# Kernel tuning notes

Measured on AMD Instinct MI355X. Metric: run time of the kernel, lower is better.

The kernel has to match this reference:

```python
import jax, jax.numpy as jnp
import numpy as np

EMBED = 128   # embed_dims
NCAM = 6      # cameras per sample
FH, FW = 6, 12  # per-camera feature map size (same at every scale here)
THRESH = 0.01   # opacity threshold (GaussianRenderer.threshold)
SIZES = [25, 50, 100, 200]  # int(200 * 2**(s - 4 + 1)) for s in 0..3


def setup_inputs() -> dict:
    key = jax.random.key(0)
    ks = jax.random.split(key, 16)
    inp = {}
    for s in range(4):
        kf, km, ku, ko = ks[4 * s:4 * s + 4]
        inp[f"features{s}"] = jax.random.normal(kf, (NCAM, EMBED, FH, FW), dtype=jnp.float32)
        # means in the BEV range (-50, 50) meters
        inp[f"means{s}"] = jax.random.uniform(km, (NCAM, FH, FW, 3), minval=-50.0, maxval=50.0, dtype=jnp.float32)
        # PSD 3x3 uncertainty (covariance) per gaussian
        L = jax.random.normal(ku, (NCAM, FH, FW, 3, 3), dtype=jnp.float32)
        inp[f"uncert{s}"] = jnp.einsum('...ij,...kj->...ik', L, L) * 2.0 + jnp.eye(3, dtype=jnp.float32)
        inp[f"opac{s}"] = jax.random.uniform(ko, (NCAM, 1, FH, FW), dtype=jnp.float32)
    inp["b"] = 1
    inp["n"] = NCAM
    return inp


def _render_scale(feat, mean, unc, opac, H, W, b):
    # feat: [(b n), d, h, w]; mean: [(b n), h, w, 3]; unc: [(b n), h, w, 3, 3]; opac: [(b n), 1, h, w]
    bn, d, h, w = feat.shape
    N = (bn // b) * h * w
    f = feat.transpose(0, 2, 3, 1).reshape(b, N, d)          # b (n h w) d
    m = mean.reshape(b, N, 3)
    c9 = unc.reshape(b, N, 9)                                # flatten(-2,-1)
    # pack [xx, xy, xz, yy, yz, zz] then clamp(min=1)
    c6 = jnp.maximum(jnp.concatenate([c9[:, :, 0:3], c9[:, :, 4:6], c9[:, :, 8:9]], axis=-1), 1.0)
    o = opac.transpose(0, 2, 3, 1).reshape(b, N)

    # orthographic BEV projection: pix_row = -sh*y + H/2, pix_col = -sw*x + W/2
    sh = H / 100.0
    sw = W / 100.0
    pr = -sh * m[:, :, 1] + H / 2.0
    pc = -sw * m[:, :, 0] + W / 2.0

    # 2D covariance = J Sigma J^T with J = [[0,-sh,0],[-sw,0,0]]; +0.3 pixel dilation
    va = sh * sh * c6[:, :, 3] + 0.3   # row-row (from Sigma_yy)
    vb = sh * sw * c6[:, :, 1]         # row-col (from Sigma_xy)
    vc = sw * sw * c6[:, :, 0] + 0.3   # col-col (from Sigma_xx)
    det = va * vc - vb * vb

    rows = jnp.arange(H, dtype=feat.dtype)
    cols = jnp.arange(W, dtype=feat.dtype)
    dr = pr[:, :, None, None] - rows[None, None, :, None]    # [b,N,H,1]
    dc = pc[:, :, None, None] - cols[None, None, None, :]    # [b,N,1,W]

    power = (-0.5 * (vc[:, :, None, None] * dr * dr + va[:, :, None, None] * dc * dc)
             + vb[:, :, None, None] * dr * dc) / det[:, :, None, None]   # [b,N,H,W]

    keep = (o > THRESH) & (det > 0.0)                        # mask-gather expressed as alpha zeroing
    alpha = jnp.minimum(0.99, o[:, :, None, None] * jnp.exp(jnp.minimum(power, 0.0)))
    alpha = jnp.where(keep[:, :, None, None] & (power <= 0.0) & (alpha >= 1.0 / 255.0), alpha, 0.0)

    # front-to-back alpha compositing in gaussian order (depth is identically 0 in BEV)
    A = alpha.reshape(b, N, H * W)
    T = jnp.cumprod(1.0 - A, axis=1)
    T_excl = jnp.concatenate([jnp.ones_like(T[:, :1]), T[:, :-1]], axis=1)
    out = jnp.einsum('bnp,bnd->bdp', A * T_excl, f).reshape(b, d, H, W)  # bg color is zeros

    num_g = (o > THRESH).astype(feat.dtype).sum(1).mean()
    return out, num_g


def reference(features0, features1, features2, features3,
              means0, means1, means2, means3,
              uncert0, uncert1, uncert2, uncert3,
              opac0, opac1, opac2, opac3, b, n):
    feats = [features0, features1, features2, features3]
    means = [means0, means1, means2, means3]
    uncs = [uncert0, uncert1, uncert2, uncert3]
    ops = [opac0, opac1, opac2, opac3]
    outs = []
    num_gaussians = jnp.float32(0.0)
    for s in range(4):
        o, g = _render_scale(feats[s], means[s], uncs[s], ops[s], SIZES[s], SIZES[s], b)
        outs.append(o)
        num_gaussians = num_gaussians + g
    return (outs[0], outs[1], outs[2], outs[3], num_gaussians)
```

## Files before the change

kernel.cpp:

```cpp
#include <hip/hip_runtime.h>

#define NCAM   6
#define FHW    72
#define EMBED  128
#define NG     432
#define THRESH 0.01f
#define AMIN   (1.0f/255.0f)
#define NTILES 891
#define TC     432

struct Args {
    const float* feat[4];
    const float* mean[4];
    const float* unc[4];
    const float* opac[4];
};

__device__ __forceinline__ void tile_decode(int g, int& s, int& H, int& band, int& chunk)
{
    int tb;
    if (g < 14)       { s = 0; H = 25;  tb = g;       chunk = tb & 1;  band = tb >> 1; }
    else if (g < 66)  { s = 1; H = 50;  tb = g - 14;  chunk = tb & 3;  band = tb >> 2; }
    else if (g < 241) { s = 2; H = 100; tb = g - 66;  band = tb / 7;   chunk = tb - band * 7; }
    else              { s = 3; H = 200; tb = g - 241; band = tb / 13;  chunk = tb - band * 13; }
}

__global__ __launch_bounds__(256) void prep(Args a, float* __restrict__ ft,
                                            int* __restrict__ tlen,
                                            float4* __restrict__ p4a,
                                            float4* __restrict__ p4b,
                                            float* __restrict__ out)
{
    int b = blockIdx.x, t = threadIdx.x;
    if (b < NTILES) {
        __shared__ int s_cnt[8];
        int g = b;
        int s, H, band, chunk;
        tile_decode(g, s, H, band, chunk);
        int lane = t & 63, wv = t >> 6;
        float sh = H * 0.01f;
        float r0f = (float)(band * 4), r1f = (float)min(band * 4 + 3, H - 1);
        float c0f = (float)(chunk * 16), c1f = (float)min(chunk * 16 + 15, H - 1);
        const float* mean = a.mean[s];
        const float* unc  = a.unc[s];
        const float* opac = a.opac[s];

        bool v_act[2]; int v_rnk[2];
        float v_pr[2], v_pc[2], v_qa[2], v_qb[2], v_qc[2], v_ok[2];
        #pragma unroll
        for (int pp = 0; pp < 2; pp++) {
            int j = pp * 256 + t;
            bool act = false;
            float pr = 0.f, pc = 0.f, qa = 0.f, qb = 0.f, qc = 0.f, ok = 0.f;
            if (j < NG) {
                float m0 = mean[j*3+0], m1 = mean[j*3+1];
                float u00 = fmaxf(unc[j*9+0], 1.f);
                float u01 = fmaxf(unc[j*9+1], 1.f);
                float u11 = fmaxf(unc[j*9+4], 1.f);
                float op = opac[j];
                pr = -sh*m1 + H*0.5f;
                pc = -sh*m0 + H*0.5f;
                float va = sh*sh*u11 + 0.3f;
                float vb = sh*sh*u01;
                float vc = sh*sh*u00 + 0.3f;
                float det = va*vc - vb*vb;
                if (op > THRESH && det > 0.f) {
                    float inv = 1.f/det;
                    qa = 0.5f*vc*inv;
                    qc = 0.5f*va*inv;
                    qb = vb*inv;
                    ok = op;
                    float thr = __logf(255.f*op);
                    float Rr = sqrtf(2.f*va*thr) + 1e-2f;
                    float Rc = sqrtf(2.f*vc*thr) + 1e-2f;
                    act = (pr >= r0f-Rr) && (pr <= r1f+Rr) &&
                          (pc >= c0f-Rc) && (pc <= c1f+Rc);
                }
            }
            unsigned long long m = __ballot(act);
            v_act[pp] = act;
            v_rnk[pp] = __popcll(m & ((1ull << lane) - 1ull));
            v_pr[pp]=pr; v_pc[pp]=pc; v_qa[pp]=qa; v_qb[pp]=qb; v_qc[pp]=qc; v_ok[pp]=ok;
            if (lane == 0) s_cnt[pp*4 + wv] = __popcll(m);
        }
        __syncthreads();
        int c8[8];
        #pragma unroll
        for (int i = 0; i < 8; i++) c8[i] = s_cnt[i];
        int len = 0;
        #pragma unroll
        for (int i = 0; i < 8; i++) len += c8[i];
        #pragma unroll
        for (int pp = 0; pp < 2; pp++) {
            int slot = pp*4 + wv;
            int pre = 0;
            #pragma unroll
            for (int i = 0; i < 8; i++) pre += (i < slot) ? c8[i] : 0;
            if (v_act[pp]) {
                int idx = g*TC + pre + v_rnk[pp];
                int j = pp * 256 + t;
                unsigned off = (unsigned)((s*NG + j) * EMBED);
                p4a[idx] = make_float4(v_pr[pp], v_pc[pp], v_qa[pp], v_qb[pp]);
                p4b[idx] = make_float4(v_qc[pp], v_ok[pp], __uint_as_float(off), 0.f);
            }
        }
        if (t == 0) tlen[g] = len;
    } else if (b < NTILES + 24) {
        __shared__ float l[EMBED * 73];
        int sc = b - NTILES;
        int s = sc / NCAM, cam = sc - s * NCAM;
        const float* src = a.feat[s] + cam * (EMBED * FHW);
        for (int i = t; i < EMBED * FHW; i += 256) {
            int d = i / FHW, hw = i - d * FHW;
            l[d * 73 + hw] = src[i];
        }
        __syncthreads();
        float* dst = ft + (s * NG + cam * FHW) * EMBED;
        for (int e = t; e < EMBED * FHW; e += 256) {
            int hw = e >> 7, d = e & 127;
            dst[hw * EMBED + d] = l[d * 73 + hw];
        }
    } else {
        __shared__ float red[256];
        float c = 0.f;
        for (int s = 0; s < 4; s++)
            for (int i = t; i < NG; i += 256)
                c += (a.opac[s][i] > THRESH) ? 1.f : 0.f;
        red[t] = c;
        __syncthreads();
        for (int st = 128; st > 0; st >>= 1) {
            if (t < st) red[t] += red[t + st];
            __syncthreads();
        }
        if (t == 0) out[6800000] = red[0];
    }
}

__global__ __launch_bounds__(256) void render(const float* __restrict__ ft,
                                              const int* __restrict__ tlen,
                                              const float4* __restrict__ p4a,
                                              const float4* __restrict__ p4b,
                                              float* __restrict__ out)
{
    __shared__ float s_T[4][64];
    __shared__ float s_part[3][64][33];

    int bb = blockIdx.x, t = threadIdx.x;
    int g = bb >> 2, chq = bb & 3;
    int s, H, band, chunk;
    tile_decode(g, s, H, band, chunk);
    int P = H * H;
    float* o = out + ((s == 0) ? 0 : (s == 1) ? 80000 : (s == 2) ? 400000 : 1680000);
    int lane = t & 63;
    int wv = __builtin_amdgcn_readfirstlane(t >> 6);
    int ch0 = chq * 32;
    int len = tlen[g];
    int qlen = (len + 3) >> 2;
    int k0 = wv * qlen, k1 = min(k0 + qlen, len);
    int base = g * TC;
    int row = band*4 + (lane >> 4), col = chunk*16 + (lane & 15);
    float frow = (float)row, fcol = (float)col;

    float acc[32];
    #pragma unroll
    for (int i = 0; i < 32; i++) acc[i] = 0.f;
    float T = 1.f;

    if (k0 < k1) {
        float4 A = p4a[base + k0];
        float4 B = p4b[base + k0];
        for (int k = k0; k < k1; k++) {
            unsigned off = __builtin_amdgcn_readfirstlane(__float_as_uint(B.z));
            const float* fr = ft + off + ch0;
            float4 f0 = *reinterpret_cast<const float4*>(fr);
            float4 f1 = *reinterpret_cast<const float4*>(fr + 4);
            float4 f2 = *reinterpret_cast<const float4*>(fr + 8);
            float4 f3 = *reinterpret_cast<const float4*>(fr + 12);
            float4 f4 = *reinterpret_cast<const float4*>(fr + 16);
            float4 f5 = *reinterpret_cast<const float4*>(fr + 20);
            float4 f6 = *reinterpret_cast<const float4*>(fr + 24);
            float4 f7 = *reinterpret_cast<const float4*>(fr + 28);
            int kn = (k + 1 < k1) ? k + 1 : k;
            float4 An = p4a[base + kn];
            float4 Bn = p4b[base + kn];
            float dr = A.x - frow, dc = A.y - fcol;
            float pw = A.w*dr*dc - A.z*dr*dr - B.x*dc*dc;
            float aL = 0.f;
            if (pw <= 0.f) {
                aL = fminf(B.y * __expf(pw), 0.99f);
                aL = (aL >= AMIN) ? aL : 0.f;
            }
            float w = aL * T;
            T *= (1.f - aL);
            acc[0]  += w * f0.x; acc[1]  += w * f0.y; acc[2]  += w * f0.z; acc[3]  += w * f0.w;
            acc[4]  += w * f1.x; acc[5]  += w * f1.y; acc[6]  += w * f1.z; acc[7]  += w * f1.w;
            acc[8]  += w * f2.x; acc[9]  += w * f2.y; acc[10] += w * f2.z; acc[11] += w * f2.w;
            acc[12] += w * f3.x; acc[13] += w * f3.y; acc[14] += w * f3.z; acc[15] += w * f3.w;
            acc[16] += w * f4.x; acc[17] += w * f4.y; acc[18] += w * f4.z; acc[19] += w * f4.w;
            acc[20] += w * f5.x; acc[21] += w * f5.y; acc[22] += w * f5.z; acc[23] += w * f5.w;
            acc[24] += w * f6.x; acc[25] += w * f6.y; acc[26] += w * f6.z; acc[27] += w * f6.w;
            acc[28] += w * f7.x; acc[29] += w * f7.y; acc[30] += w * f7.z; acc[31] += w * f7.w;
            A = An; B = Bn;
        }
    }

    s_T[wv][lane] = T;
    __syncthreads();
    if (wv > 0) {
        float pref = s_T[0][lane];
        if (wv > 1) pref *= s_T[1][lane];
        if (wv > 2) pref *= s_T[2][lane];
        #pragma unroll
        for (int i = 0; i < 32; i++)
            s_part[wv-1][lane][i] = acc[i] * pref;
    }
    __syncthreads();
    if (wv == 0 && row < H && col < H) {
        int pp = row * H + col;
        #pragma unroll
        for (int i = 0; i < 32; i++) {
            float v = acc[i] + s_part[0][lane][i] + s_part[1][lane][i]
                             + s_part[2][lane][i];
            o[(ch0 + i) * P + pp] = v;
        }
    }
}

extern "C" void kernel_launch(void* const* d_in, const int* in_sizes, int n_in,
                              void* d_out, int out_size, void* d_ws, size_t ws_size,
                              hipStream_t stream)
{
    Args a;
    for (int s = 0; s < 4; s++) {
        a.feat[s] = (const float*)d_in[4 * s + 0];
        a.mean[s] = (const float*)d_in[4 * s + 1];
        a.unc[s]  = (const float*)d_in[4 * s + 2];
        a.opac[s] = (const float*)d_in[4 * s + 3];
    }
    float* ws = (float*)d_ws;
    float*  ft   = ws;
    int*    tlen = (int*)(ws + 221184);
    float4* p4a  = (float4*)(ws + 222080);
    float4* p4b  = p4a + NTILES * TC;

    prep<<<NTILES + 24 + 1, 256, 0, stream>>>(a, ft, tlen, p4a, p4b, (float*)d_out);
    render<<<NTILES * 4, 256, 0, stream>>>(ft, tlen, p4a, p4b, (float*)d_out);
}
```

Before: 27.12 us.

## Rebalance render work split across k-sections and channel quarters per scale

```diff
diff --git a/kernel.cpp b/kernel.cpp
--- a/kernel.cpp
+++ b/kernel.cpp
@@ -136,27 +136,34 @@
     }
 }
 
-__global__ __launch_bounds__(256) void render(const float* __restrict__ ft,
+__global__ __launch_bounds__(512) void render(const float* __restrict__ ft,
                                               const int* __restrict__ tlen,
                                               const float4* __restrict__ p4a,
                                               const float4* __restrict__ p4b,
                                               float* __restrict__ out)
 {
-    __shared__ float s_T[4][64];
-    __shared__ float s_part[3][64][33];
+    __shared__ float s_T[8][64];
+    __shared__ float s_part[7][64][33];
 
     int bb = blockIdx.x, t = threadIdx.x;
-    int g = bb >> 2, chq = bb & 3;
+    int lane = t & 63;
+    int wv = __builtin_amdgcn_readfirstlane(t >> 6);
+    int g, chq, ksec, ksections;
+    bool longscale;
+    if (bb < 264) {
+        longscale = true;  g = bb >> 2;        chq = bb & 3;  ksec = wv;      ksections = 8;
+    } else {
+        longscale = false; g = 66 + (bb - 264); chq = wv >> 1; ksec = wv & 1;  ksections = 2;
+    }
+
     int s, H, band, chunk;
     tile_decode(g, s, H, band, chunk);
     int P = H * H;
     float* o = out + ((s == 0) ? 0 : (s == 1) ? 80000 : (s == 2) ? 400000 : 1680000);
-    int lane = t & 63;
-    int wv = __builtin_amdgcn_readfirstlane(t >> 6);
+    int len = tlen[g];
+    int ql = (len + ksections - 1) / ksections;
+    int k0 = min(ksec * ql, len), k1 = min(k0 + ql, len);
     int ch0 = chq * 32;
-    int len = tlen[g];
-    int qlen = (len + 3) >> 2;
-    int k0 = wv * qlen, k1 = min(k0 + qlen, len);
     int base = g * TC;
     int row = band*4 + (lane >> 4), col = chunk*16 + (lane & 15);
     float frow = (float)row, fcol = (float)col;
@@ -204,24 +211,51 @@
         }
     }
 
-    s_T[wv][lane] = T;
-    __syncthreads();
-    if (wv > 0) {
-        float pref = s_T[0][lane];
-        if (wv > 1) pref *= s_T[1][lane];
-        if (wv > 2) pref *= s_T[2][lane];
-        #pragma unroll
-        for (int i = 0; i < 32; i++)
-            s_part[wv-1][lane][i] = acc[i] * pref;
-    }
-    __syncthreads();
-    if (wv == 0 && row < H && col < H) {
-        int pp = row * H + col;
-        #pragma unroll
-        for (int i = 0; i < 32; i++) {
-            float v = acc[i] + s_part[0][lane][i] + s_part[1][lane][i]
-                             + s_part[2][lane][i];
-            o[(ch0 + i) * P + pp] = v;
+    bool inb = (row < H) && (col < H);
+    int pp = row * H + col;
+
+    if (longscale) {
+        s_T[wv][lane] = T;
+        __syncthreads();
+        if (wv > 0) {
+            float pref = s_T[0][lane];
+            #pragma unroll
+            for (int q = 1; q < 7; q++)
+                if (q < wv) pref *= s_T[q][lane];
+            #pragma unroll
+            for (int i = 0; i < 32; i++)
+                s_part[wv-1][lane][i] = acc[i] * pref;
+        }
+        __syncthreads();
+        if (wv == 0 && inb) {
+            #pragma unroll
+            for (int i = 0; i < 32; i++) {
+                float v = acc[i];
+                #pragma unroll
+                for (int q = 0; q < 7; q++) v += s_part[q][lane][i];
+                o[(ch0 + i) * P + pp] = v;
+            }
+        }
+    } else {
+        if (wv == 0) {
+            #pragma unroll
+            for (int i = 0; i < 64; i += 64) ;
+            s_T[0][lane] = T;
+        }
+        __syncthreads();
+        if (ksec == 1) {
+            float pref = s_T[0][lane];
+            #pragma unroll
+            for (int i = 0; i < 32; i++)
+                s_part[chq][lane][i] = acc[i] * pref;
+        }
+        __syncthreads();
+        if (ksec == 0 && inb) {
+            #pragma unroll
+            for (int i = 0; i < 32; i++) {
+                float v = acc[i] + s_part[chq][lane][i];
+                o[(ch0 + i) * P + pp] = v;
+            }
         }
     }
 }
@@ -244,5 +278,5 @@
     float4* p4b  = p4a + NTILES * TC;
 
     prep<<<NTILES + 24 + 1, 256, 0, stream>>>(a, ft, tlen, p4a, p4b, (float*)d_out);
-    render<<<NTILES * 4, 256, 0, stream>>>(ft, tlen, p4a, p4b, (float*)d_out);
-}
+    render<<<264 + 825, 512, 0, stream>>>(ft, tlen, p4a, p4b, (float*)d_out);
+}
```

New measurement: 29.88 us. +10.2%, slower.
